# Kernel tuning notes

Hardware: AMD Instinct MI355X
Metric: run time of the kernel (lower is better)

## Reference

```python
import jax, jax.numpy as jnp
import numpy as np

B, C, T, H, W = 2, 512, 8, 16, 16
NUM_HEADS = 8
HEAD_DIM = C // NUM_HEADS


def setup_inputs() -> dict:
    key = jax.random.key(0)
    ks = jax.random.split(key, 6)
    x = jax.random.normal(ks[0], (B, C, T, H, W), dtype=jnp.float32)
    # LayerNorm params
    ln_w = jnp.ones((C,), dtype=jnp.float32)
    ln_b = jnp.zeros((C,), dtype=jnp.float32)
    # 1x1x1 Conv3d == per-token linear; weight stored [out, in]
    w_qkv = jax.random.normal(ks[1], (3 * C, C), dtype=jnp.float32) * (1.0 / np.sqrt(C))
    b_qkv = jnp.zeros((3 * C,), dtype=jnp.float32)
    w_proj = jax.random.normal(ks[2], (C, C), dtype=jnp.float32) * (1.0 / np.sqrt(C))
    b_proj = jnp.zeros((C,), dtype=jnp.float32)
    return {"x": x, "ln_w": ln_w, "ln_b": ln_b, "w_qkv": w_qkv,
            "b_qkv": b_qkv, "w_proj": w_proj, "b_proj": b_proj}


def reference(x, ln_w, ln_b, w_qkv, b_qkv, w_proj, b_proj):
    Bx, Cx, Tx, Hx, Wx = x.shape
    N = Tx * Hx * Wx
    scale = HEAD_DIM ** -0.5

    # [B,C,T,H,W] -> [B,N,C]
    x_flat = jnp.transpose(x, (0, 2, 3, 4, 1)).reshape(Bx, N, Cx)

    # LayerNorm over channels
    mu = jnp.mean(x_flat, axis=-1, keepdims=True)
    var = jnp.var(x_flat, axis=-1, keepdims=True)
    x_flat = (x_flat - mu) * jax.lax.rsqrt(var + 1e-5) * ln_w + ln_b

    # QKV (1x1x1 conv == linear). Output channel layout: [3, heads, head_dim]
    qkv = jnp.einsum('bnc,oc->bno', x_flat, w_qkv) + b_qkv  # [B,N,3C]
    qkv = qkv.reshape(Bx, N, 3, NUM_HEADS, HEAD_DIM)
    qkv = jnp.transpose(qkv, (2, 0, 3, 1, 4))  # [3,B,heads,N,head_dim]
    q, k, v = qkv[0], qkv[1], qkv[2]

    attn = jnp.einsum('bhnd,bhmd->bhnm', q, k) * scale
    attn = jax.nn.softmax(attn, axis=-1)
    x_attn = jnp.einsum('bhnm,bhmd->bhnd', attn, v)  # [B,heads,N,head_dim]
    x_attn = jnp.transpose(x_attn, (0, 2, 1, 3)).reshape(Bx, N, Cx)

    # proj (1x1x1 conv == linear)
    x_attn = jnp.einsum('bnc,oc->bno', x_attn, w_proj) + b_proj

    # NOTE: residual is on the *normalized* x_flat (as in the original module)
    x_out = x_flat + x_attn
    x_out = x_out.reshape(Bx, Tx, Hx, Wx, Cx)
    return jnp.transpose(x_out, (0, 4, 1, 2, 3))  # [B,C,T,H,W]
```

## Files before the change

### kernel.cpp

```cpp
#include <hip/hip_runtime.h>
#include <hip/hip_bf16.h>

#define BB 2
#define CC 512
#define NN 2048
#define NHEADS 8
#define HDIM 64
#define NSPLIT 2
#define KVHALF 1024

typedef __attribute__((ext_vector_type(8))) __bf16 bf16x8;
typedef __attribute__((ext_vector_type(4))) __bf16 bf16x4;
typedef __attribute__((ext_vector_type(2))) __bf16 bf16x2;
typedef __attribute__((ext_vector_type(4))) float f32x4;

#define QSCALE 0.18033688f

__global__ __launch_bounds__(256) void ln_stats_kernel(
    const float* __restrict__ x, float* __restrict__ mu, float* __restrict__ rstd) {
  __shared__ float rs[16][16];
  __shared__ float rq[16][16];
  int tl = threadIdx.x & 15;
  int cg = threadIdx.x >> 4;
  int tok = blockIdx.x * 16 + tl;
  int b = tok >> 11;
  int n = tok & (NN - 1);
  const float* xp = x + (size_t)b * CC * NN + n;
  float s = 0.f, ss = 0.f;
  int c0 = cg * 32;
#pragma unroll 8
  for (int c = c0; c < c0 + 32; ++c) {
    float v = xp[(size_t)c * NN];
    s += v;
    ss += v * v;
  }
  rs[cg][tl] = s;
  rq[cg][tl] = ss;
  __syncthreads();
  if (threadIdx.x < 16) {
    int t = threadIdx.x;
    float S = 0.f, SS = 0.f;
#pragma unroll
    for (int gidx = 0; gidx < 16; ++gidx) {
      S += rs[gidx][t];
      SS += rq[gidx][t];
    }
    float m = S * (1.0f / CC);
    float var = SS * (1.0f / CC) - m * m;
    int tk = blockIdx.x * 16 + t;
    mu[tk] = m;
    rstd[tk] = rsqrtf(var + 1e-5f);
  }
}

__global__ __launch_bounds__(256) void ln_transpose_kernel(
    const float* __restrict__ x, const float* __restrict__ mu,
    const float* __restrict__ rstd, const float* __restrict__ lnw,
    const float* __restrict__ lnb, __bf16* __restrict__ xln_t) {
  __shared__ float Xs[64][68];
  int n0 = blockIdx.x * 64;
  int c0 = blockIdx.y * 64;
  int b = blockIdx.z;
  int tid = threadIdx.x;
#pragma unroll
  for (int l = 0; l < 4; ++l) {
    int e = tid + 256 * l;
    int row = e >> 4, c4 = e & 15;
    float4 v = *(const float4*)&x[((size_t)b * CC + c0 + row) * NN + n0 + c4 * 4];
    *(float4*)&Xs[row][c4 * 4] = v;
  }
  __syncthreads();
  int sr = tid >> 2;
  int sc = (tid & 3) * 16;
  int tok = b * NN + n0 + sr;
  float mun = mu[tok], rsn = rstd[tok];
  __bf16 outv[16];
#pragma unroll
  for (int j = 0; j < 16; ++j) {
    int c = c0 + sc + j;
    outv[j] = (__bf16)((Xs[sc + j][sr] - mun) * rsn * lnw[c] + lnb[c]);
  }
  __bf16* dst = &xln_t[((size_t)b * NN + n0 + sr) * CC + c0 + sc];
  *(bf16x8*)&dst[0] = *(bf16x8*)&outv[0];
  *(bf16x8*)&dst[8] = *(bf16x8*)&outv[8];
}

__global__ __launch_bounds__(256) void qkv_mfma_kernel(
    const __bf16* __restrict__ xln_t, const float* __restrict__ w,
    const float* __restrict__ bias, __bf16* __restrict__ qt,
    __bf16* __restrict__ kt, __bf16* __restrict__ vbf) {
  __shared__ __align__(16) __bf16 As[2][64][68];
  __shared__ __align__(16) __bf16 Bs[2][128][68];
  int n0 = blockIdx.x * 128;
  bool swap = blockIdx.y < 16;
  int m0 = swap ? blockIdx.y * 64 : 1024 + ((int)blockIdx.y - 16) * 64;
  int b = blockIdx.z;
  int tid = threadIdx.x;
  int wid = tid >> 6, lane = tid & 63;
  int g = lane >> 4, c = lane & 15;
  int wr = wid >> 1, wc = wid & 1;
  const __bf16* xln = xln_t + (size_t)b * NN * CC;
  int arow = tid >> 4, ac4 = tid & 15;
  int brow = tid >> 3, bc8 = tid & 7;

  float4 wA[4];
  bf16x8 xB[4];
  auto LOADREGS = [&](int k0) {
#pragma unroll
    for (int l = 0; l < 4; ++l)
      wA[l] = *(const float4*)&w[(size_t)(m0 + arow + 16 * l) * CC + k0 + ac4 * 4];
#pragma unroll
    for (int l = 0; l < 4; ++l)
      xB[l] = *(const bf16x8*)&xln[(size_t)(n0 + brow + 32 * l) * CC + k0 + bc8 * 8];
  };
  auto STORELDS = [&](int buf) {
#pragma unroll
    for (int l = 0; l < 4; ++l) {
      bf16x4 pk = {(__bf16)wA[l].x, (__bf16)wA[l].y, (__bf16)wA[l].z,
                   (__bf16)wA[l].w};
      *(bf16x4*)&As[buf][arow + 16 * l][ac4 * 4] = pk;
    }
#pragma unroll
    for (int l = 0; l < 4; ++l)
      *(bf16x8*)&Bs[buf][brow + 32 * l][bc8 * 8] = xB[l];
  };

  LOADREGS(0);
  STORELDS(0);
  __syncthreads();
  f32x4 acc[2][4] = {};
  for (int ktile = 0; ktile < 8; ++ktile) {
    int cur = ktile & 1;
    if (ktile < 7) LOADREGS((ktile + 1) * 64);
#pragma unroll
    for (int hh = 0; hh < 2; ++hh) {
      bf16x8 af[2], bfr[4];
#pragma unroll
      for (int mi = 0; mi < 2; ++mi)
        af[mi] = *(const bf16x8*)&As[cur][wr * 32 + mi * 16 + c][hh * 32 + g * 8];
#pragma unroll
      for (int nj = 0; nj < 4; ++nj)
        bfr[nj] = *(const bf16x8*)&Bs[cur][wc * 64 + nj * 16 + c][hh * 32 + g * 8];
      if (swap) {
#pragma unroll
        for (int mi = 0; mi < 2; ++mi)
#pragma unroll
          for (int nj = 0; nj < 4; ++nj)
            acc[mi][nj] = __builtin_amdgcn_mfma_f32_16x16x32_bf16(
                bfr[nj], af[mi], acc[mi][nj], 0, 0, 0);
      } else {
#pragma unroll
        for (int mi = 0; mi < 2; ++mi)
#pragma unroll
          for (int nj = 0; nj < 4; ++nj)
            acc[mi][nj] = __builtin_amdgcn_mfma_f32_16x16x32_bf16(
                af[mi], bfr[nj], acc[mi][nj], 0, 0, 0);
      }
    }
    if (ktile < 7) STORELDS(cur ^ 1);
    __syncthreads();
  }
  if (swap) {
    int obase = m0 + wr * 32;
    int sec = obase >> 9;
    int osec = obase & 511;
    int head = osec >> 6;
    int dbase = osec & 63;
    __bf16* dst = (sec == 0 ? qt : kt) + (size_t)(b * NHEADS + head) * NN * HDIM;
    float scl = (sec == 0) ? QSCALE : 1.0f;
#pragma unroll
    for (int mi = 0; mi < 2; ++mi) {
      float bo = bias[obase + mi * 16 + c];
      int d = dbase + mi * 16 + c;
#pragma unroll
      for (int nj = 0; nj < 4; ++nj)
#pragma unroll
        for (int r = 0; r < 4; ++r) {
          int n = n0 + wc * 64 + nj * 16 + 4 * g + r;
          dst[(size_t)n * HDIM + d] = (__bf16)((acc[mi][nj][r] + bo) * scl);
        }
    }
  } else {
#pragma unroll
    for (int mi = 0; mi < 2; ++mi)
#pragma unroll
      for (int r = 0; r < 4; ++r) {
        int o = m0 + wr * 32 + mi * 16 + 4 * g + r;
        int ch = o - 1024;
        float bo = bias[o];
#pragma unroll
        for (int nj = 0; nj < 4; ++nj) {
          int n = n0 + wc * 64 + nj * 16 + c;
          vbf[((size_t)b * CC + ch) * NN + n] = (__bf16)(acc[mi][nj][r] + bo);
        }
      }
  }
}

__global__ __launch_bounds__(512, 4) void attn_mfma_kernel(
    const __bf16* __restrict__ qt, const __bf16* __restrict__ ktg,
    const __bf16* __restrict__ vbf, float* __restrict__ opart,
    float* __restrict__ ml) {
  __shared__ __align__(16) __bf16 Kb[2][64][72];
  __shared__ __align__(16) __bf16 Vb[2][64][72];
  __shared__ __align__(16) __bf16 Ps[128][72];
  int tid = threadIdx.x;
  int wid = tid >> 6, lane = tid & 63;
  int g = lane >> 4, c = lane & 15;
  int n0 = blockIdx.x * 128;
  int h = blockIdx.y;
  int b = blockIdx.z >> 1, split = blockIdx.z & 1;
  int bh = b * NHEADS + h;
  const __bf16* qbase = qt + ((size_t)bh * NN + n0) * HDIM;
  const __bf16* kbase = ktg + ((size_t)bh * NN + split * KVHALF) * HDIM;
  const __bf16* vbase = vbf + ((size_t)b * CC + h * HDIM) * NN + split * KVHALF;

  int sr = tid >> 3, sc = (tid & 7) * 8;
  bf16x8 kr = *(const bf16x8*)(kbase + (size_t)sr * HDIM + sc);
  bf16x8 vr = *(const bf16x8*)(vbase + (size_t)sr * NN + sc);
  bf16x8 aq0 = *(const bf16x8*)(qbase + (size_t)(wid * 16 + c) * HDIM + g * 8);
  bf16x8 aq1 = *(const bf16x8*)(qbase + (size_t)(wid * 16 + c) * HDIM + 32 + g * 8);
  *(bf16x8*)&Kb[0][sr][sc] = kr;
  *(bf16x8*)&Vb[0][sr][sc] = vr;

  f32x4 O[4] = {};
  float m_ = -1e30f;
  float l_ = 0.f;
  __syncthreads();

  for (int t = 0; t < KVHALF / 64; ++t) {
    int cur = t & 1;
    bool pf = (t + 1 < KVHALF / 64);
    int mt = (t + 1) * 64;
    if (pf) {
      kr = *(const bf16x8*)(kbase + (size_t)(mt + sr) * HDIM + sc);
      vr = *(const bf16x8*)(vbase + (size_t)sr * NN + mt + sc);
    }
    f32x4 st[4];
    __builtin_amdgcn_s_setprio(1);
#pragma unroll
    for (int t4 = 0; t4 < 4; ++t4) {
      bf16x8 bk0 = *(const bf16x8*)&Kb[cur][t4 * 16 + c][g * 8];
      bf16x8 bk1 = *(const bf16x8*)&Kb[cur][t4 * 16 + c][32 + g * 8];
      f32x4 acc = {0.f, 0.f, 0.f, 0.f};
      acc = __builtin_amdgcn_mfma_f32_16x16x32_bf16(bk0, aq0, acc, 0, 0, 0);
      acc = __builtin_amdgcn_mfma_f32_16x16x32_bf16(bk1, aq1, acc, 0, 0, 0);
      st[t4] = acc;
    }
    __builtin_amdgcn_s_setprio(0);
    float pm = st[0][0];
#pragma unroll
    for (int t4 = 0; t4 < 4; ++t4)
#pragma unroll
      for (int r = 0; r < 4; ++r) pm = fmaxf(pm, st[t4][r]);
    pm = fmaxf(pm, __shfl_xor(pm, 16));
    pm = fmaxf(pm, __shfl_xor(pm, 32));
    if (!__all(pm <= m_ + 8.0f)) {
      float mn = fmaxf(m_, pm);
      float fs = exp2f(m_ - mn);
      m_ = mn;
      l_ *= fs;
#pragma unroll
      for (int dt = 0; dt < 4; ++dt)
#pragma unroll
        for (int r = 0; r < 4; ++r) O[dt][r] *= fs;
    }
    float ps = 0.f;
#pragma unroll
    for (int t4 = 0; t4 < 4; ++t4) {
      float p0 = exp2f(st[t4][0] - m_);
      float p1 = exp2f(st[t4][1] - m_);
      float p2 = exp2f(st[t4][2] - m_);
      float p3 = exp2f(st[t4][3] - m_);
      ps += (p0 + p1) + (p2 + p3);
      bf16x4 quad = {(__bf16)p0, (__bf16)p1, (__bf16)p2, (__bf16)p3};
      *(bf16x4*)&Ps[wid * 16 + c][t4 * 16 + 4 * g] = quad;
    }
    l_ += ps;
    bf16x8 ap0 = *(const bf16x8*)&Ps[wid * 16 + c][g * 8];
    bf16x8 ap1 = *(const bf16x8*)&Ps[wid * 16 + c][32 + g * 8];
    __builtin_amdgcn_s_setprio(1);
#pragma unroll
    for (int dt = 0; dt < 4; ++dt) {
      bf16x8 bv0 = *(const bf16x8*)&Vb[cur][dt * 16 + c][g * 8];
      bf16x8 bv1 = *(const bf16x8*)&Vb[cur][dt * 16 + c][32 + g * 8];
      O[dt] = __builtin_amdgcn_mfma_f32_16x16x32_bf16(bv0, ap0, O[dt], 0, 0, 0);
      O[dt] = __builtin_amdgcn_mfma_f32_16x16x32_bf16(bv1, ap1, O[dt], 0, 0, 0);
    }
    __builtin_amdgcn_s_setprio(0);
    if (pf) {
      *(bf16x8*)&Kb[cur ^ 1][sr][sc] = kr;
      *(bf16x8*)&Vb[cur ^ 1][sr][sc] = vr;
    }
    __syncthreads();
  }
  float lt = l_ + __shfl_xor(l_, 16);
  lt += __shfl_xor(lt, 32);
  size_t prow = ((size_t)(split * BB + b) * NHEADS + h) * NN + (n0 + wid * 16 + c);
#pragma unroll
  for (int dt = 0; dt < 4; ++dt)
    *(f32x4*)&opart[prow * HDIM + dt * 16 + 4 * g] = O[dt];
  if (lane < 16) {
    float2 mlv = {m_, lt};
    *(float2*)&ml[prow * 2] = mlv;
  }
}

__global__ __launch_bounds__(256) void attn_combine_kernel(
    const float* __restrict__ opart, const float* __restrict__ ml,
    __bf16* __restrict__ xa_t) {
  int t = threadIdx.x;
  int row_local = t >> 4;
  int dq = (t & 15) * 4;
  int R = blockIdx.x * 16 + row_local;
  int n = R & (NN - 1);
  int bh = R >> 11;
  int b = bh >> 3, h = bh & 7;
  size_t p0 = ((size_t)(0 * BB + b) * NHEADS + h) * NN + n;
  size_t p1 = ((size_t)(1 * BB + b) * NHEADS + h) * NN + n;
  float m0 = ml[p0 * 2], l0 = ml[p0 * 2 + 1];
  float m1 = ml[p1 * 2], l1 = ml[p1 * 2 + 1];
  float m = fmaxf(m0, m1);
  float w0 = exp2f(m0 - m), w1 = exp2f(m1 - m);
  float linv = 1.0f / (l0 * w0 + l1 * w1);
  float4 o0 = *(const float4*)&opart[p0 * HDIM + dq];
  float4 o1 = *(const float4*)&opart[p1 * HDIM + dq];
  bf16x4 pk = {(__bf16)((o0.x * w0 + o1.x * w1) * linv),
               (__bf16)((o0.y * w0 + o1.y * w1) * linv),
               (__bf16)((o0.z * w0 + o1.z * w1) * linv),
               (__bf16)((o0.w * w0 + o1.w * w1) * linv)};
  *(bf16x4*)&xa_t[((size_t)b * NN + n) * CC + h * HDIM + dq] = pk;
}

__global__ __launch_bounds__(256) void proj_mfma_kernel(
    const __bf16* __restrict__ xa_t, const float* __restrict__ w,
    const float* __restrict__ bias, const float* __restrict__ x,
    const float* __restrict__ mu, const float* __restrict__ rstd,
    const float* __restrict__ lnw, const float* __restrict__ lnb,
    float* __restrict__ out) {
  __shared__ __align__(16) __bf16 As[2][64][68];
  __shared__ __align__(16) __bf16 Bs[2][64][68];
  int n0 = blockIdx.x * 64;
  int m0 = blockIdx.y * 64;
  int b = blockIdx.z;
  int tid = threadIdx.x;
  int wid = tid >> 6, lane = tid & 63;
  int g = lane >> 4, c = lane & 15;
  int wr = wid >> 1, wc = wid & 1;
  const __bf16* xab = xa_t + (size_t)b * NN * CC;
  int arow = tid >> 4, ac4 = tid & 15;
  int brow = tid >> 3, bc8 = tid & 7;

  float4 wA[4];
  bf16x8 xB[2];
  auto LOADREGS = [&](int k0) {
#pragma unroll
    for (int l = 0; l < 4; ++l)
      wA[l] = *(const float4*)&w[(size_t)(m0 + arow + 16 * l) * CC + k0 + ac4 * 4];
#pragma unroll
    for (int l = 0; l < 2; ++l)
      xB[l] = *(const bf16x8*)&xab[(size_t)(n0 + brow + 32 * l) * CC + k0 + bc8 * 8];
  };
  auto STORELDS = [&](int buf) {
#pragma unroll
    for (int l = 0; l < 4; ++l) {
      bf16x4 pk = {(__bf16)wA[l].x, (__bf16)wA[l].y, (__bf16)wA[l].z,
                   (__bf16)wA[l].w};
      *(bf16x4*)&As[buf][arow + 16 * l][ac4 * 4] = pk;
    }
#pragma unroll
    for (int l = 0; l < 2; ++l)
      *(bf16x8*)&Bs[buf][brow + 32 * l][bc8 * 8] = xB[l];
  };

  LOADREGS(0);
  STORELDS(0);
  __syncthreads();
  f32x4 acc[2][2] = {};
  for (int ktile = 0; ktile < 8; ++ktile) {
    int cur = ktile & 1;
    if (ktile < 7) LOADREGS((ktile + 1) * 64);
#pragma unroll
    for (int hh = 0; hh < 2; ++hh) {
      bf16x8 af[2], bfr[2];
#pragma unroll
      for (int mi = 0; mi < 2; ++mi)
        af[mi] = *(const bf16x8*)&As[cur][wr * 32 + mi * 16 + c][hh * 32 + g * 8];
#pragma unroll
      for (int nj = 0; nj < 2; ++nj)
        bfr[nj] = *(const bf16x8*)&Bs[cur][wc * 32 + nj * 16 + c][hh * 32 + g * 8];
#pragma unroll
      for (int mi = 0; mi < 2; ++mi)
#pragma unroll
        for (int nj = 0; nj < 2; ++nj)
          acc[mi][nj] = __builtin_amdgcn_mfma_f32_16x16x32_bf16(
              af[mi], bfr[nj], acc[mi][nj], 0, 0, 0);
    }
    if (ktile < 7) STORELDS(cur ^ 1);
    __syncthreads();
  }
#pragma unroll
  for (int mi = 0; mi < 2; ++mi)
#pragma unroll
    for (int r = 0; r < 4; ++r) {
      int o = m0 + wr * 32 + mi * 16 + 4 * g + r;
      float bo = bias[o], gw = lnw[o], gb = lnb[o];
#pragma unroll
      for (int nj = 0; nj < 2; ++nj) {
        int n = n0 + wc * 32 + nj * 16 + c;
        int tok = b * NN + n;
        float xv = x[((size_t)b * CC + o) * NN + n];
        float xlnv = (xv - mu[tok]) * rstd[tok] * gw + gb;
        out[((size_t)b * CC + o) * NN + n] = acc[mi][nj][r] + bo + xlnv;
      }
    }
}

extern "C" void kernel_launch(void* const* d_in, const int* in_sizes, int n_in,
                              void* d_out, int out_size, void* d_ws, size_t ws_size,
                              hipStream_t stream) {
  const float* x = (const float*)d_in[0];
  const float* lnw = (const float*)d_in[1];
  const float* lnb = (const float*)d_in[2];
  const float* wqkv = (const float*)d_in[3];
  const float* bqkv = (const float*)d_in[4];
  const float* wproj = (const float*)d_in[5];
  const float* bproj = (const float*)d_in[6];
  float* out = (float*)d_out;
  (void)in_sizes; (void)n_in; (void)out_size; (void)ws_size;

  char* wsb = (char*)d_ws;
  float* mu = (float*)wsb;
  float* rstd = mu + 4096;
  const size_t HSZ = (size_t)BB * NHEADS * NN * HDIM;
  __bf16* qt = (__bf16*)(wsb + 32768);
  __bf16* kt = qt + HSZ;
  __bf16* vbf = kt + HSZ;
  __bf16* xa_t = vbf + HSZ;
  __bf16* xln_t = xa_t + HSZ;
  float* opart = (float*)xln_t;
  float* ml = (float*)(wsb + 32768 + 4 * HSZ * sizeof(__bf16) +
                       (size_t)NSPLIT * HSZ * sizeof(float));

  hipLaunchKernelGGL(ln_stats_kernel, dim3(256), dim3(256), 0, stream, x, mu, rstd);
  hipLaunchKernelGGL(ln_transpose_kernel, dim3(32, 8, 2), dim3(256), 0, stream,
                     x, mu, rstd, lnw, lnb, xln_t);
  hipLaunchKernelGGL(qkv_mfma_kernel, dim3(16, 24, 2), dim3(256), 0, stream,
                     xln_t, wqkv, bqkv, qt, kt, vbf);
  hipLaunchKernelGGL(attn_mfma_kernel, dim3(16, 8, 4), dim3(512), 0, stream,
                     qt, kt, vbf, opart, ml);
  hipLaunchKernelGGL(attn_combine_kernel, dim3(2048), dim3(256), 0, stream,
                     opart, ml, xa_t);
  hipLaunchKernelGGL(proj_mfma_kernel, dim3(32, 8, 2), dim3(256), 0, stream,
                     xa_t, wproj, bproj, x, mu, rstd, lnw, lnb, out);
}
```

Before: 80.04 us.

## Restructure attention kernel: direct-to-LDS loads, swizzled tiles, register-resident P, 2 query groups

```diff
diff --git a/kernel.cpp b/kernel.cpp
--- a/kernel.cpp
+++ b/kernel.cpp
@@ -13,6 +13,9 @@
 typedef __attribute__((ext_vector_type(4))) __bf16 bf16x4;
 typedef __attribute__((ext_vector_type(2))) __bf16 bf16x2;
 typedef __attribute__((ext_vector_type(4))) float f32x4;
+
+typedef const __attribute__((address_space(1))) unsigned int guint;
+typedef __attribute__((address_space(3))) unsigned int suint;
 
 #define QSCALE 0.18033688f
 
@@ -197,13 +200,12 @@
   }
 }
 
-__global__ __launch_bounds__(512, 4) void attn_mfma_kernel(
+__global__ __launch_bounds__(256, 4) void attn_mfma_kernel(
     const __bf16* __restrict__ qt, const __bf16* __restrict__ ktg,
     const __bf16* __restrict__ vbf, float* __restrict__ opart,
     float* __restrict__ ml) {
-  __shared__ __align__(16) __bf16 Kb[2][64][72];
-  __shared__ __align__(16) __bf16 Vb[2][64][72];
-  __shared__ __align__(16) __bf16 Ps[128][72];
+  __shared__ __align__(16) __bf16 Kb[2][64][64];
+  __shared__ __align__(16) __bf16 Vb[2][64][64];
   int tid = threadIdx.x;
   int wid = tid >> 6, lane = tid & 63;
   int g = lane >> 4, c = lane & 15;
@@ -215,94 +217,122 @@
   const __bf16* kbase = ktg + ((size_t)bh * NN + split * KVHALF) * HDIM;
   const __bf16* vbase = vbf + ((size_t)b * CC + h * HDIM) * NN + split * KVHALF;
 
-  int sr = tid >> 3, sc = (tid & 7) * 8;
-  bf16x8 kr = *(const bf16x8*)(kbase + (size_t)sr * HDIM + sc);
-  bf16x8 vr = *(const bf16x8*)(vbase + (size_t)sr * NN + sc);
-  bf16x8 aq0 = *(const bf16x8*)(qbase + (size_t)(wid * 16 + c) * HDIM + g * 8);
-  bf16x8 aq1 = *(const bf16x8*)(qbase + (size_t)(wid * 16 + c) * HDIM + 32 + g * 8);
-  *(bf16x8*)&Kb[0][sr][sc] = kr;
-  *(bf16x8*)&Vb[0][sr][sc] = vr;
-
-  f32x4 O[4] = {};
-  float m_ = -1e30f;
-  float l_ = 0.f;
+  int l7 = lane & 7, l3 = lane >> 3;
+  int xr = (l7 ^ l3) * 8;
+  auto STAGE = [&](int buf, int mt) {
+#pragma unroll
+    for (int j = 0; j < 2; ++j) {
+      int r = wid * 16 + 8 * j + l3;
+      int gr = (r & 0x20) | (((r >> 2) & 3) << 3) | (((r >> 4) & 1) << 2) | (r & 3);
+      const __bf16* ksrc = kbase + (size_t)(mt + gr) * HDIM + xr;
+      __builtin_amdgcn_global_load_lds((guint*)ksrc,
+                                       (suint*)&Kb[buf][wid * 16 + 8 * j][0],
+                                       16, 0, 0);
+      const __bf16* vsrc = vbase + (size_t)r * NN + mt + xr;
+      __builtin_amdgcn_global_load_lds((guint*)vsrc,
+                                       (suint*)&Vb[buf][wid * 16 + 8 * j][0],
+                                       16, 0, 0);
+    }
+  };
+
+  STAGE(0, 0);
+  bf16x8 aq[2][2];
+#pragma unroll
+  for (int qg = 0; qg < 2; ++qg) {
+    const __bf16* qp = qbase + (size_t)(wid * 32 + qg * 16 + c) * HDIM;
+    aq[qg][0] = *(const bf16x8*)(qp + g * 8);
+    aq[qg][1] = *(const bf16x8*)(qp + 32 + g * 8);
+  }
+  f32x4 O[2][4] = {};
+  float m_[2] = {-1e30f, -1e30f};
+  float l_[2] = {0.f, 0.f};
+  int cxor = (c & 7);
   __syncthreads();
 
   for (int t = 0; t < KVHALF / 64; ++t) {
     int cur = t & 1;
-    bool pf = (t + 1 < KVHALF / 64);
-    int mt = (t + 1) * 64;
-    if (pf) {
-      kr = *(const bf16x8*)(kbase + (size_t)(mt + sr) * HDIM + sc);
-      vr = *(const bf16x8*)(vbase + (size_t)sr * NN + mt + sc);
-    }
-    f32x4 st[4];
+    if (t + 1 < KVHALF / 64) STAGE(cur ^ 1, (t + 1) * 64);
+    f32x4 st[2][4];
     __builtin_amdgcn_s_setprio(1);
 #pragma unroll
     for (int t4 = 0; t4 < 4; ++t4) {
-      bf16x8 bk0 = *(const bf16x8*)&Kb[cur][t4 * 16 + c][g * 8];
-      bf16x8 bk1 = *(const bf16x8*)&Kb[cur][t4 * 16 + c][32 + g * 8];
-      f32x4 acc = {0.f, 0.f, 0.f, 0.f};
-      acc = __builtin_amdgcn_mfma_f32_16x16x32_bf16(bk0, aq0, acc, 0, 0, 0);
-      acc = __builtin_amdgcn_mfma_f32_16x16x32_bf16(bk1, aq1, acc, 0, 0, 0);
-      st[t4] = acc;
+      bf16x8 bk0 = *(const bf16x8*)&Kb[cur][t4 * 16 + c][(g ^ cxor) * 8];
+      bf16x8 bk1 = *(const bf16x8*)&Kb[cur][t4 * 16 + c][((4 + g) ^ cxor) * 8];
+#pragma unroll
+      for (int qg = 0; qg < 2; ++qg) {
+        f32x4 acc = {0.f, 0.f, 0.f, 0.f};
+        acc = __builtin_amdgcn_mfma_f32_16x16x32_bf16(bk0, aq[qg][0], acc, 0, 0, 0);
+        acc = __builtin_amdgcn_mfma_f32_16x16x32_bf16(bk1, aq[qg][1], acc, 0, 0, 0);
+        st[qg][t4] = acc;
+      }
     }
     __builtin_amdgcn_s_setprio(0);
-    float pm = st[0][0];
-#pragma unroll
-    for (int t4 = 0; t4 < 4; ++t4)
-#pragma unroll
-      for (int r = 0; r < 4; ++r) pm = fmaxf(pm, st[t4][r]);
-    pm = fmaxf(pm, __shfl_xor(pm, 16));
-    pm = fmaxf(pm, __shfl_xor(pm, 32));
-    if (!__all(pm <= m_ + 8.0f)) {
-      float mn = fmaxf(m_, pm);
-      float fs = exp2f(m_ - mn);
-      m_ = mn;
-      l_ *= fs;
-#pragma unroll
-      for (int dt = 0; dt < 4; ++dt)
-#pragma unroll
-        for (int r = 0; r < 4; ++r) O[dt][r] *= fs;
-    }
-    float ps = 0.f;
-#pragma unroll
-    for (int t4 = 0; t4 < 4; ++t4) {
-      float p0 = exp2f(st[t4][0] - m_);
-      float p1 = exp2f(st[t4][1] - m_);
-      float p2 = exp2f(st[t4][2] - m_);
-      float p3 = exp2f(st[t4][3] - m_);
-      ps += (p0 + p1) + (p2 + p3);
-      bf16x4 quad = {(__bf16)p0, (__bf16)p1, (__bf16)p2, (__bf16)p3};
-      *(bf16x4*)&Ps[wid * 16 + c][t4 * 16 + 4 * g] = quad;
-    }
-    l_ += ps;
-    bf16x8 ap0 = *(const bf16x8*)&Ps[wid * 16 + c][g * 8];
-    bf16x8 ap1 = *(const bf16x8*)&Ps[wid * 16 + c][32 + g * 8];
+    bf16x8 pa[2][2];
+#pragma unroll
+    for (int qg = 0; qg < 2; ++qg) {
+      float pm = st[qg][0][0];
+#pragma unroll
+      for (int t4 = 0; t4 < 4; ++t4)
+#pragma unroll
+        for (int r = 0; r < 4; ++r) pm = fmaxf(pm, st[qg][t4][r]);
+      pm = fmaxf(pm, __shfl_xor(pm, 16));
+      pm = fmaxf(pm, __shfl_xor(pm, 32));
+      if (!__all(pm <= m_[qg] + 8.0f)) {
+        float mn = fmaxf(m_[qg], pm);
+        float fs = exp2f(m_[qg] - mn);
+        m_[qg] = mn;
+        l_[qg] *= fs;
+#pragma unroll
+        for (int dt = 0; dt < 4; ++dt)
+#pragma unroll
+          for (int r = 0; r < 4; ++r) O[qg][dt][r] *= fs;
+      }
+      float ps = 0.f;
+#pragma unroll
+      for (int t4 = 0; t4 < 4; ++t4) {
+        float p0 = exp2f(st[qg][t4][0] - m_[qg]);
+        float p1 = exp2f(st[qg][t4][1] - m_[qg]);
+        float p2 = exp2f(st[qg][t4][2] - m_[qg]);
+        float p3 = exp2f(st[qg][t4][3] - m_[qg]);
+        ps += (p0 + p1) + (p2 + p3);
+        bf16x8* pt = &pa[qg][t4 >> 1];
+        int o4 = (t4 & 1) * 4;
+        (*pt)[o4 + 0] = (__bf16)p0;
+        (*pt)[o4 + 1] = (__bf16)p1;
+        (*pt)[o4 + 2] = (__bf16)p2;
+        (*pt)[o4 + 3] = (__bf16)p3;
+      }
+      l_[qg] += ps;
+    }
     __builtin_amdgcn_s_setprio(1);
 #pragma unroll
     for (int dt = 0; dt < 4; ++dt) {
-      bf16x8 bv0 = *(const bf16x8*)&Vb[cur][dt * 16 + c][g * 8];
-      bf16x8 bv1 = *(const bf16x8*)&Vb[cur][dt * 16 + c][32 + g * 8];
-      O[dt] = __builtin_amdgcn_mfma_f32_16x16x32_bf16(bv0, ap0, O[dt], 0, 0, 0);
-      O[dt] = __builtin_amdgcn_mfma_f32_16x16x32_bf16(bv1, ap1, O[dt], 0, 0, 0);
+      bf16x8 bv0 = *(const bf16x8*)&Vb[cur][dt * 16 + c][(g ^ cxor) * 8];
+      bf16x8 bv1 = *(const bf16x8*)&Vb[cur][dt * 16 + c][((4 + g) ^ cxor) * 8];
+#pragma unroll
+      for (int qg = 0; qg < 2; ++qg) {
+        O[qg][dt] = __builtin_amdgcn_mfma_f32_16x16x32_bf16(bv0, pa[qg][0],
+                                                            O[qg][dt], 0, 0, 0);
+        O[qg][dt] = __builtin_amdgcn_mfma_f32_16x16x32_bf16(bv1, pa[qg][1],
+                                                            O[qg][dt], 0, 0, 0);
+      }
     }
     __builtin_amdgcn_s_setprio(0);
-    if (pf) {
-      *(bf16x8*)&Kb[cur ^ 1][sr][sc] = kr;
-      *(bf16x8*)&Vb[cur ^ 1][sr][sc] = vr;
-    }
     __syncthreads();
   }
-  float lt = l_ + __shfl_xor(l_, 16);
-  lt += __shfl_xor(lt, 32);
-  size_t prow = ((size_t)(split * BB + b) * NHEADS + h) * NN + (n0 + wid * 16 + c);
-#pragma unroll
-  for (int dt = 0; dt < 4; ++dt)
-    *(f32x4*)&opart[prow * HDIM + dt * 16 + 4 * g] = O[dt];
-  if (lane < 16) {
-    float2 mlv = {m_, lt};
-    *(float2*)&ml[prow * 2] = mlv;
+#pragma unroll
+  for (int qg = 0; qg < 2; ++qg) {
+    float lt = l_[qg] + __shfl_xor(l_[qg], 16);
+    lt += __shfl_xor(lt, 32);
+    size_t prow = ((size_t)(split * BB + b) * NHEADS + h) * NN +
+                  (n0 + wid * 32 + qg * 16 + c);
+#pragma unroll
+    for (int dt = 0; dt < 4; ++dt)
+      *(f32x4*)&opart[prow * HDIM + dt * 16 + 4 * g] = O[qg][dt];
+    if (lane < 16) {
+      float2 mlv = {m_[qg], lt};
+      *(float2*)&ml[prow * 2] = mlv;
+    }
   }
 }
 
@@ -447,7 +477,7 @@
                      x, mu, rstd, lnw, lnb, xln_t);
   hipLaunchKernelGGL(qkv_mfma_kernel, dim3(16, 24, 2), dim3(256), 0, stream,
                      xln_t, wqkv, bqkv, qt, kt, vbf);
-  hipLaunchKernelGGL(attn_mfma_kernel, dim3(16, 8, 4), dim3(512), 0, stream,
+  hipLaunchKernelGGL(attn_mfma_kernel, dim3(16, 8, 4), dim3(256), 0, stream,
                      qt, kt, vbf, opart, ml);
   hipLaunchKernelGGL(attn_combine_kernel, dim3(2048), dim3(256), 0, stream,
                      opart, ml, xa_t);
```

New measurement: 82.46 us. 1.03x slower.
